# Optimization experiments

Measured on AMD Instinct MI355X. Metric: run time of the kernel, lower is better.

## Reference

```python
import jax, jax.numpy as jnp
import numpy as np

B, N, NC = 16, 25200, 80
CONF_THRES = 0.25
IOU_THRES = 0.45
MAX_DET = 300
MAX_WH = 7680.0   # yolov5 per-class box offset for class-aware NMS
TOPK = 1024       # pre-NMS candidate cap (fixed-shape stand-in for yolov5 max_nms)


def setup_inputs():
    key = jax.random.key(0)
    k1, k2 = jax.random.split(key)
    # xywh in pixel units (640x640 image, boxes up to ~120 px); obj/cls confidences in [0,1]
    xywh = jax.random.uniform(k1, (B, N, 4), dtype=jnp.float32) * jnp.array([640.0, 640.0, 120.0, 120.0], jnp.float32)
    conf = jax.random.uniform(k2, (B, N, 1 + NC), dtype=jnp.float32)
    return {"YOLOoutput": jnp.concatenate([xywh, conf], axis=-1)}


def _xywh2xyxy(x):
    cx, cy, w, h = x[..., 0], x[..., 1], x[..., 2], x[..., 3]
    return jnp.stack([cx - w / 2, cy - h / 2, cx + w / 2, cy + h / 2], axis=-1)


def _pairwise_iou(a, b):
    # a, b: [K,4] xyxy -> [K,K]
    lt = jnp.maximum(a[:, None, :2], b[None, :, :2])
    rb = jnp.minimum(a[:, None, 2:], b[None, :, 2:])
    wh = jnp.maximum(rb - lt, 0.0)
    inter = wh[..., 0] * wh[..., 1]
    area_a = (a[:, 2] - a[:, 0]) * (a[:, 3] - a[:, 1])
    area_b = (b[:, 2] - b[:, 0]) * (b[:, 3] - b[:, 1])
    return inter / (area_a[:, None] + area_b[None, :] - inter + 1e-7)


def _nms_single(pred):
    # pred: [N, 5+NC]
    obj = pred[:, 4]
    cls_conf = pred[:, 5:] * obj[:, None]      # conf = obj_conf * cls_conf (yolov5)
    conf = jnp.max(cls_conf, axis=-1)
    j = jnp.argmax(cls_conf, axis=-1)
    valid = (obj > CONF_THRES) & (conf > CONF_THRES)
    box = _xywh2xyxy(pred[:, :4])
    scores = jnp.where(valid, conf, -1.0)      # invalid candidates sink to bottom
    top_scores, idx = jax.lax.top_k(scores, TOPK)
    b = box[idx]                               # [TOPK,4]
    c = j[idx].astype(box.dtype)
    boxes_off = b + (c * MAX_WH)[:, None]      # class-aware NMS via per-class offset
    valid_k = top_scores > 0.0
    iou = _pairwise_iou(boxes_off, boxes_off)
    ar = jnp.arange(TOPK)

    def body(i, supp):
        active = jnp.logical_not(supp[i])
        return supp | (active & (iou[i] > IOU_THRES) & (ar > i))

    supp = jax.lax.fori_loop(0, TOPK, body, jnp.logical_not(valid_k))
    keep = valid_k & jnp.logical_not(supp)
    fs, fi = jax.lax.top_k(jnp.where(keep, top_scores, -1.0), MAX_DET)
    dv = fs > 0.0
    det_box = b[fi] * dv[:, None]              # zero out padded rows
    det = jnp.concatenate(
        [det_box, jnp.where(dv, fs, 0.0)[:, None], (c[fi] * dv)[:, None]], axis=-1
    )                                          # [MAX_DET, 6] = x1,y1,x2,y2,conf,cls
    return det, dv


def reference(YOLOoutput):
    det, dvalid = jax.vmap(_nms_single)(YOLOoutput)   # [B,MAX_DET,6], [B,MAX_DET]
    scores = det[..., 4]
    mean_conf = jnp.max(scores, axis=1)               # = 0 when image has no detections
    n = dvalid.sum(axis=1)
    terms = jnp.abs(det[..., 0:2] - det[..., 2:4]) * scores[..., None]  # padded rows are 0
    s = terms.sum(axis=(1, 2))
    wh = jnp.where(n > 0, s / (2.0 * jnp.maximum(n, 1)), 0.0)  # mean over n*2 elements
    conf_addition = mean_conf.sum() / B
    w_and_h = wh.sum() / B
    return conf_addition, w_and_h, det[2]
```

## Files before the change

### kernel.cpp

```cpp
#include <hip/hip_runtime.h>
#include <hip/hip_bf16.h>

typedef unsigned long long u64;
typedef unsigned int u32;

#define BATCH 16
#define NANCH 25200
#define NCLS 80
#define NFEAT 85
#define TOPK 1024
#define MAXDET 300
#define CONF_T 0.25f
#define IOU_T 0.45f
#define MAX_WH 7680.0f

#define GRP 16
#define GRPB (GRP * NFEAT * 4)
#define NGRP (NANCH / GRP)

__device__ __forceinline__ void gload_lds16(const void* g, void* l) {
    __builtin_amdgcn_global_load_lds(
        (const __attribute__((address_space(1))) unsigned int*)g,
        (__attribute__((address_space(3))) unsigned int*)l, 16, 0, 0);
}

__global__ __launch_bounds__(256) void score_kernel(const float* __restrict__ in,
                                                    u64* __restrict__ keys,
                                                    float* __restrict__ out) {
    __shared__ char lds[4 * GRPB];
    const int tid = threadIdx.x, wv = tid >> 6, lane = tid & 63;
    if (blockIdx.x == 0 && tid == 0) { out[0] = 0.0f; out[1] = 0.0f; }
    char* myl = lds + wv * GRPB;
    const float* myp = (const float*)myl + (lane >> 2) * NFEAT;
    const int a = lane >> 2, q = lane & 3;
    const int wave_id = (blockIdx.x << 2) | wv;
    const int nwaves = gridDim.x << 2;
    for (int g = wave_id; g < BATCH * NGRP; g += nwaves) {
        const int b = g / NGRP;
        const int a0 = (g - b * NGRP) * GRP;
        const char* gbase = (const char*)(in + ((size_t)b * NANCH + a0) * NFEAT);
#pragma unroll
        for (int r = 0; r < 6; ++r) {
            const int myb = (r << 10) + lane * 16;
            if (myb < GRPB) gload_lds16(gbase + myb, myl + (r << 10));
        }
        asm volatile("s_waitcnt vmcnt(0)" ::: "memory");
        __builtin_amdgcn_sched_barrier(0);
        float obj = myp[4];
        float best = -1e30f;
        int bj = 0;
#pragma unroll
        for (int k = 0; k < 20; ++k) {
            float v = myp[5 + q * 20 + k] * obj;
            if (v > best) { best = v; bj = q * 20 + k; }
        }
#pragma unroll
        for (int d = 1; d < 4; d <<= 1) {
            float ob = __shfl_xor(best, d, 64);
            int oj = __shfl_xor(bj, d, 64);
            if (ob > best || (ob == best && oj < bj)) { best = ob; bj = oj; }
        }
        if (q == 0) {
            bool valid = (obj > CONF_T) && (best > CONF_T);
            float sc = valid ? best : -1.0f;
            u32 sb = __float_as_uint(sc);
            u32 ord = sb ^ ((sb & 0x80000000u) ? 0xFFFFFFFFu : 0x80000000u);
            int idx = a0 + a;
            keys[(size_t)b * NANCH + idx] =
                ((u64)ord << 32) | ((u64)((u32)(idx ^ 0xFFFF) & 0xFFFFu) << 8) | (u64)bj;
        }
    }
}

__global__ __launch_bounds__(1024) void select_topk(const u64* __restrict__ keys,
                                                    const float* __restrict__ in,
                                                    float4* __restrict__ box4,
                                                    float4* __restrict__ boxoff4,
                                                    float* __restrict__ score,
                                                    float* __restrict__ cls,
                                                    u64* __restrict__ vmask) {
    const int b = blockIdx.x, tid = threadIdx.x;
    const int lane = tid & 63, wv = tid >> 6;
    const u64* kb = keys + (size_t)b * NANCH;
    const ulonglong2* kb2 = (const ulonglong2*)kb;
    __shared__ u32 wcnt[16][17];
    __shared__ u32 tot[17];
    __shared__ u32 s_prefix12, s_cnt;
    __shared__ u64 buf[2048];

    u32 myc = 0;
    for (int n = tid; n < 12600; n += 1024) {
        ulonglong2 kk = kb2[n];
        u32 b0 = (u32)(kk.x >> 52);
        u32 b1 = (u32)(kk.y >> 52);
        u32 c0 = (b0 == 0x407u) ? 16u : (b0 - 0xBE8u);
        u32 c1 = (b1 == 0x407u) ? 16u : (b1 - 0xBE8u);
#pragma unroll
        for (u32 k = 0; k < 17; ++k) {
            u64 m0 = __ballot(c0 == k);
            u64 m1 = __ballot(c1 == k);
            if (lane == (int)k) myc += (u32)__popcll(m0) + (u32)__popcll(m1);
        }
    }
    if (lane < 17) wcnt[wv][lane] = myc;
    if (tid == 0) s_cnt = 0u;
    __syncthreads();
    if (tid < 17) {
        u32 t = 0;
#pragma unroll
        for (int w = 0; w < 16; ++w) t += wcnt[w][tid];
        tot[tid] = t;
    }
    __syncthreads();
    if (tid == 0) {
        u32 acc = 0; u32 p = 0x407u;
        for (int k = 15; k >= 0; --k) {
            if (acc < (u32)TOPK && acc + tot[k] >= (u32)TOPK) p = 0xBE8u + (u32)k;
            acc += tot[k];
        }
        if (acc < (u32)TOPK) p = 0x407u;
        s_prefix12 = p;
    }
    __syncthreads();
    const u32 p12 = s_prefix12;
    for (int n = tid; n < 12600; n += 1024) {
        ulonglong2 kk = kb2[n];
        if ((u32)(kk.x >> 52) > p12) {
            u32 pos = atomicAdd(&s_cnt, 1u);
            if (pos < 2048u) buf[pos] = kk.x;
        }
        if ((u32)(kk.y >> 52) > p12) {
            u32 pos = atomicAdd(&s_cnt, 1u);
            if (pos < 2048u) buf[pos] = kk.y;
        }
    }
    __syncthreads();
    for (int n = tid; n < 12600; n += 1024) {
        ulonglong2 kk = kb2[n];
        if ((u32)(kk.x >> 52) == p12) {
            u32 pos = atomicAdd(&s_cnt, 1u);
            if (pos < 2048u) buf[pos] = kk.x;
        }
        if ((u32)(kk.y >> 52) == p12) {
            u32 pos = atomicAdd(&s_cnt, 1u);
            if (pos < 2048u) buf[pos] = kk.y;
        }
    }
    __syncthreads();
    u32 cnt = s_cnt; if (cnt > 2048u) cnt = 2048u;
    for (int n = (int)cnt + tid; n < 2048; n += 1024) buf[n] = 0ull;
    __syncthreads();

    const int base = wv * 128;
    u64 r0 = buf[base + lane], r1 = buf[base + 64 + lane];
    for (int k2 = 2; k2 <= 128; k2 <<= 1) {
        const bool d0 = (((base + lane) & k2) == 0);
        const bool d1 = (((base + 64 + lane) & k2) == 0);
        for (int jj = (k2 >> 1); jj >= 1; jj >>= 1) {
            if (jj == 64) {
                u64 mx = r0 > r1 ? r0 : r1, mn = r0 > r1 ? r1 : r0;
                r0 = d0 ? mx : mn; r1 = d0 ? mn : mx;
            } else {
                const bool up = (lane & jj) != 0;
                u64 v0 = __shfl_xor(r0, jj, 64);
                u64 v1 = __shfl_xor(r1, jj, 64);
                const bool km0 = (d0 != up), km1 = (d1 != up);
                r0 = km0 ? (r0 > v0 ? r0 : v0) : (r0 < v0 ? r0 : v0);
                r1 = km1 ? (r1 > v1 ? r1 : v1) : (r1 < v1 ? r1 : v1);
            }
        }
    }
    for (int k2 = 256; k2 <= 2048; k2 <<= 1) {
        buf[base + lane] = r0; buf[base + 64 + lane] = r1;
        __syncthreads();
        for (int jj = (k2 >> 1); jj >= 128; jj >>= 1) {
            int i = ((tid & ~(jj - 1)) << 1) | (tid & (jj - 1));
            int part = i | jj;
            u64 a = buf[i], c = buf[part];
            bool sw = ((i & k2) == 0) ? (a < c) : (a > c);
            if (sw) { buf[i] = c; buf[part] = a; }
            __syncthreads();
        }
        r0 = buf[base + lane]; r1 = buf[base + 64 + lane];
        const bool d0 = (((base + lane) & k2) == 0);
        for (int jj = 64; jj >= 1; jj >>= 1) {
            if (jj == 64) {
                u64 mx = r0 > r1 ? r0 : r1, mn = r0 > r1 ? r1 : r0;
                r0 = d0 ? mx : mn; r1 = d0 ? mn : mx;
            } else {
                const bool up = (lane & jj) != 0;
                u64 v0 = __shfl_xor(r0, jj, 64);
                u64 v1 = __shfl_xor(r1, jj, 64);
                const bool km = (d0 != up);
                r0 = km ? (r0 > v0 ? r0 : v0) : (r0 < v0 ? r0 : v0);
                r1 = km ? (r1 > v1 ? r1 : v1) : (r1 < v1 ? r1 : v1);
            }
        }
    }
    buf[base + lane] = r0; buf[base + 64 + lane] = r1;
    __syncthreads();

    u64 k = buf[tid];
    u32 ord = (u32)(k >> 32);
    u32 sb = (ord & 0x80000000u) ? (ord ^ 0x80000000u) : ~ord;
    float sc = __uint_as_float(sb);
    int idx = (int)((((u32)(k >> 8)) & 0xFFFFu) ^ 0xFFFFu);
    int j = (int)(k & 0xFFu);
    const float* pr = in + ((size_t)b * NANCH + idx) * NFEAT;
    float cx = pr[0], cy = pr[1], ww = pr[2], hh = pr[3];
    float x1 = cx - ww / 2.0f, y1 = cy - hh / 2.0f;
    float x2 = cx + ww / 2.0f, y2 = cy + hh / 2.0f;
    float c = (float)j;
    float cm = c * MAX_WH;
    box4[b * TOPK + tid]    = make_float4(x1, y1, x2, y2);
    boxoff4[b * TOPK + tid] = make_float4(x1 + cm, y1 + cm, x2 + cm, y2 + cm);
    score[b * TOPK + tid] = sc;
    cls[b * TOPK + tid] = c;
    u64 bal = __ballot(sc > 0.0f);
    if ((tid & 63) == 0) vmask[b * 16 + (tid >> 6)] = bal;
}

__global__ __launch_bounds__(256) void iou_mask(const float4* __restrict__ boxoff4,
                                                u64* __restrict__ M) {
    __shared__ float4 sbx[TOPK];
    const int b = blockIdx.x >> 8;
    const int rb = blockIdx.x & 255;
    const int i = (rb << 2) | (threadIdx.x >> 6);
    const int lane = threadIdx.x & 63;
    const int tw = rb >> 4;
    const int jmin = tw << 6;
    for (int t = jmin + threadIdx.x; t < TOPK; t += 256) sbx[t] = boxoff4[b * TOPK + t];
    __syncthreads();
    const float4 A = sbx[i];
    const float areaA = (A.z - A.x) * (A.w - A.y);
    u64 myword = 0ull;
#pragma unroll 4
    for (int t = tw; t < 16; ++t) {
        int j = (t << 6) | lane;
        float4 Bx = sbx[j];
        float lx = fmaxf(A.x, Bx.x), ly = fmaxf(A.y, Bx.y);
        float rx = fminf(A.z, Bx.z), ry = fminf(A.w, Bx.w);
        float iw = fmaxf(rx - lx, 0.0f), ih = fmaxf(ry - ly, 0.0f);
        float inter = iw * ih;
        float areaB = (Bx.z - Bx.x) * (Bx.w - Bx.y);
        float iou = inter / (areaA + areaB - inter + 1e-7f);
        bool pred = (iou > IOU_T) && (j > i);
        u64 bal = __ballot(pred);
        if (lane == t) myword = bal;
    }
    if (lane < 16) M[((size_t)b * TOPK + i) * 16 + lane] = myword;
}

__global__ __launch_bounds__(512) void nms_finalize(const u64* __restrict__ M,
                                                    const u64* __restrict__ vmask,
                                                    const float4* __restrict__ box4,
                                                    const float* __restrict__ score,
                                                    const float* __restrict__ cls,
                                                    float* __restrict__ out) {
    __shared__ u64 sM[TOPK * 16];
    __shared__ u64 kw[16];
    __shared__ int wpfx[17];
    __shared__ float sdet[MAXDET * 6];
    __shared__ float s_sum, s_max;
    const int b = blockIdx.x, tid = threadIdx.x;
    {
        const ulonglong2* Ms = (const ulonglong2*)(M + (size_t)b * TOPK * 16);
        ulonglong2* Ldst = (ulonglong2*)sM;
#pragma unroll 4
        for (int t = tid; t < TOPK * 8; t += 512) Ldst[t] = Ms[t];
    }
    for (int t = tid; t < MAXDET * 6; t += 512) sdet[t] = 0.0f;
    if (tid == 0) { s_sum = 0.0f; s_max = 0.0f; }
    __syncthreads();
    if (tid < 16) {
        const int w = tid;
        const u64 vm = vmask[b * 16 + w];
        u64 supp = ~vm;
        u64 rwA[16], rwB[16];
#pragma unroll
        for (int q = 0; q < 16; ++q) rwA[q] = sM[q * 16 + w];
        for (int wb = 0; wb < 16; ++wb) {
            u64 cur = __shfl(supp, wb, 64);
#pragma unroll
            for (int c4 = 0; c4 < 4; ++c4) {
                const int rn = wb * 64 + (c4 + 1) * 16;
                if (rn < 1024) {
#pragma unroll
                    for (int q = 0; q < 16; ++q) rwB[q] = sM[(rn + q) * 16 + w];
                }
                u64 rc[16];
#pragma unroll
                for (int q = 0; q < 16; ++q) rc[q] = __shfl(rwA[q], wb, 64);
                u64 ar0 = rc[0] | rc[4] | rc[8]  | rc[12];
                u64 ar1 = rc[1] | rc[5] | rc[9]  | rc[13];
                u64 ar2 = rc[2] | rc[6] | rc[10] | rc[14];
                u64 ar3 = rc[3] | rc[7] | rc[11] | rc[15];
                const u32 intra = (u32)(((ar0 | ar1) | (ar2 | ar3)) >> (c4 * 16)) & 0xFFFFu;
                const u32 actm  = (~(u32)(cur >> (c4 * 16))) & 0xFFFFu;
                if (intra == 0u || actm == 0u) {
                    u64 s0 = 0, s1 = 0, s2 = 0, s3 = 0;
                    u64 c0 = 0, c1 = 0, c2 = 0, c3 = 0;
#pragma unroll
                    for (int q = 0; q < 16; q += 4) {
                        const u64 m0 = ((actm >> (q + 0)) & 1u) ? ~0ull : 0ull;
                        const u64 m1 = ((actm >> (q + 1)) & 1u) ? ~0ull : 0ull;
                        const u64 m2 = ((actm >> (q + 2)) & 1u) ? ~0ull : 0ull;
                        const u64 m3 = ((actm >> (q + 3)) & 1u) ? ~0ull : 0ull;
                        s0 |= rwA[q + 0] & m0;  c0 |= rc[q + 0] & m0;
                        s1 |= rwA[q + 1] & m1;  c1 |= rc[q + 1] & m1;
                        s2 |= rwA[q + 2] & m2;  c2 |= rc[q + 2] & m2;
                        s3 |= rwA[q + 3] & m3;  c3 |= rc[q + 3] & m3;
                    }
                    supp |= (s0 | s1) | (s2 | s3);
                    cur  |= (c0 | c1) | (c2 | c3);
                } else {
#pragma unroll
                    for (int q = 0; q < 16; ++q) {
                        const int ii = c4 * 16 + q;
                        const bool act = ((cur >> ii) & 1ull) == 0ull;
                        supp = act ? (supp | rwA[q]) : supp;
                        cur  = act ? (cur  | rc[q])  : cur;
                    }
                }
#pragma unroll
                for (int q = 0; q < 16; ++q) rwA[q] = rwB[q];
            }
        }
        kw[w] = vm & ~supp;
    }
    __syncthreads();
    if (tid == 0) {
        int acc = 0;
        for (int w = 0; w < 16; ++w) { wpfx[w] = acc; acc += __popcll(kw[w]); }
        wpfx[16] = acc;
    }
    __syncthreads();
    for (int r = tid; r < TOPK; r += 512) {
        int w = r >> 6, bp = r & 63;
        if ((kw[w] >> bp) & 1ull) {
            int pos = wpfx[w] + __popcll(kw[w] & ((1ull << bp) - 1ull));
            if (pos < MAXDET) {
                float4 bx = box4[b * TOPK + r];
                float s = score[b * TOPK + r];
                float c = cls[b * TOPK + r];
                sdet[pos * 6 + 0] = bx.x;
                sdet[pos * 6 + 1] = bx.y;
                sdet[pos * 6 + 2] = bx.z;
                sdet[pos * 6 + 3] = bx.w;
                sdet[pos * 6 + 4] = s;
                sdet[pos * 6 + 5] = c;
                float term = (fabsf(bx.x - bx.z) + fabsf(bx.y - bx.w)) * s;
                atomicAdd(&s_sum, term);
                if (pos == 0) s_max = s;
            }
        }
    }
    __syncthreads();
    if (tid == 0) {
        int n = wpfx[16]; if (n > MAXDET) n = MAXDET;
        float wh = (n > 0) ? (s_sum / (2.0f * (float)n)) : 0.0f;
        atomicAdd(&out[0], s_max / (float)BATCH);
        atomicAdd(&out[1], wh / (float)BATCH);
    }
    if (b == 2) {
        for (int t = tid; t < MAXDET * 6; t += 512) out[2 + t] = sdet[t];
    }
}

extern "C" void kernel_launch(void* const* d_in, const int* in_sizes, int n_in,
                              void* d_out, int out_size, void* d_ws, size_t ws_size,
                              hipStream_t stream) {
    const float* in = (const float*)d_in[0];
    float* out = (float*)d_out;
    char* ws = (char*)d_ws;

    u64*    keys     = (u64*)   (ws + 0);
    float4* boxoff4  = (float4*)(ws + 3225600);
    float4* box4     = (float4*)(ws + 3487744);
    float*  score    = (float*) (ws + 3749888);
    float*  cls      = (float*) (ws + 3815424);
    u64*    vmask    = (u64*)   (ws + 3880960);
    u64*    M        = (u64*)   (ws + 3883008);

    score_kernel<<<2048, 256, 0, stream>>>(in, keys, out);
    select_topk<<<BATCH, 1024, 0, stream>>>(keys, in, box4, boxoff4, score, cls, vmask);
    iou_mask<<<BATCH * 256, 256, 0, stream>>>(boxoff4, M);
    nms_finalize<<<BATCH, 512, 0, stream>>>(M, vmask, box4, score, cls, out);
}
```

Baseline: 279.0 us.

## Fuse select, IoU mask and NMS stages into one cooperative kernel

Replaces the three launches after scoring (top-k select, IoU mask, NMS finalize) with a single cooperative kernel of 256 blocks of 1024 threads that separates the stages with grid-wide syncs. Shared memory is overlaid through a union of the per-stage layouts. The aim is to remove kernel launch gaps and inter-kernel drain between stages. In exchange, the IoU stage runs on fewer, larger blocks, and the grid syncs plus a 1024-thread NMS block add overhead. The score kernel grid is also changed from 2048 to 2100 blocks.

Result: slower. 484.3 us (+73.6%).

```diff
diff --git a/kernel.cpp b/kernel.cpp
--- a/kernel.cpp
+++ b/kernel.cpp
@@ -1,5 +1,5 @@
 #include <hip/hip_runtime.h>
-#include <hip/hip_bf16.h>
+#include <hip/hip_cooperative_groups.h>
 
 typedef unsigned long long u64;
 typedef unsigned int u32;
@@ -72,21 +72,34 @@
     }
 }
 
-__global__ __launch_bounds__(1024) void select_topk(const u64* __restrict__ keys,
-                                                    const float* __restrict__ in,
-                                                    float4* __restrict__ box4,
-                                                    float4* __restrict__ boxoff4,
-                                                    float* __restrict__ score,
-                                                    float* __restrict__ cls,
-                                                    u64* __restrict__ vmask) {
-    const int b = blockIdx.x, tid = threadIdx.x;
+struct SmemS {
+    u32 wcnt[16][17];
+    u32 tot[17];
+    u32 s_prefix12, s_cnt;
+    u64 buf[2048];
+};
+struct SmemI { float4 sbx[TOPK]; };
+struct SmemN {
+    u64 sM[TOPK * 16];
+    u64 kw[16];
+    int wpfx[17];
+    float sdet[MAXDET * 6];
+    float s_sum, s_max;
+};
+union SmemU { SmemS s; SmemI i; SmemN n; };
+
+__device__ __forceinline__ void dev_select(int b, int tid, SmemS& sm,
+                                           const u64* __restrict__ keys,
+                                           const float* __restrict__ in,
+                                           float4* __restrict__ box4,
+                                           float4* __restrict__ boxoff4,
+                                           float* __restrict__ score,
+                                           float* __restrict__ cls,
+                                           u64* __restrict__ vmask) {
     const int lane = tid & 63, wv = tid >> 6;
     const u64* kb = keys + (size_t)b * NANCH;
     const ulonglong2* kb2 = (const ulonglong2*)kb;
-    __shared__ u32 wcnt[16][17];
-    __shared__ u32 tot[17];
-    __shared__ u32 s_prefix12, s_cnt;
-    __shared__ u64 buf[2048];
+    u64* buf = sm.buf;
 
     u32 myc = 0;
     for (int n = tid; n < 12600; n += 1024) {
@@ -102,35 +115,35 @@
             if (lane == (int)k) myc += (u32)__popcll(m0) + (u32)__popcll(m1);
         }
     }
-    if (lane < 17) wcnt[wv][lane] = myc;
-    if (tid == 0) s_cnt = 0u;
+    if (lane < 17) sm.wcnt[wv][lane] = myc;
+    if (tid == 0) sm.s_cnt = 0u;
     __syncthreads();
     if (tid < 17) {
         u32 t = 0;
 #pragma unroll
-        for (int w = 0; w < 16; ++w) t += wcnt[w][tid];
-        tot[tid] = t;
+        for (int w = 0; w < 16; ++w) t += sm.wcnt[w][tid];
+        sm.tot[tid] = t;
     }
     __syncthreads();
     if (tid == 0) {
         u32 acc = 0; u32 p = 0x407u;
         for (int k = 15; k >= 0; --k) {
-            if (acc < (u32)TOPK && acc + tot[k] >= (u32)TOPK) p = 0xBE8u + (u32)k;
-            acc += tot[k];
+            if (acc < (u32)TOPK && acc + sm.tot[k] >= (u32)TOPK) p = 0xBE8u + (u32)k;
+            acc += sm.tot[k];
         }
         if (acc < (u32)TOPK) p = 0x407u;
-        s_prefix12 = p;
-    }
-    __syncthreads();
-    const u32 p12 = s_prefix12;
+        sm.s_prefix12 = p;
+    }
+    __syncthreads();
+    const u32 p12 = sm.s_prefix12;
     for (int n = tid; n < 12600; n += 1024) {
         ulonglong2 kk = kb2[n];
         if ((u32)(kk.x >> 52) > p12) {
-            u32 pos = atomicAdd(&s_cnt, 1u);
+            u32 pos = atomicAdd(&sm.s_cnt, 1u);
             if (pos < 2048u) buf[pos] = kk.x;
         }
         if ((u32)(kk.y >> 52) > p12) {
-            u32 pos = atomicAdd(&s_cnt, 1u);
+            u32 pos = atomicAdd(&sm.s_cnt, 1u);
             if (pos < 2048u) buf[pos] = kk.y;
         }
     }
@@ -138,16 +151,16 @@
     for (int n = tid; n < 12600; n += 1024) {
         ulonglong2 kk = kb2[n];
         if ((u32)(kk.x >> 52) == p12) {
-            u32 pos = atomicAdd(&s_cnt, 1u);
+            u32 pos = atomicAdd(&sm.s_cnt, 1u);
             if (pos < 2048u) buf[pos] = kk.x;
         }
         if ((u32)(kk.y >> 52) == p12) {
-            u32 pos = atomicAdd(&s_cnt, 1u);
+            u32 pos = atomicAdd(&sm.s_cnt, 1u);
             if (pos < 2048u) buf[pos] = kk.y;
         }
     }
     __syncthreads();
-    u32 cnt = s_cnt; if (cnt > 2048u) cnt = 2048u;
+    u32 cnt = sm.s_cnt; if (cnt > 2048u) cnt = 2048u;
     for (int n = (int)cnt + tid; n < 2048; n += 1024) buf[n] = 0ull;
     __syncthreads();
 
@@ -220,6 +233,182 @@
     if ((tid & 63) == 0) vmask[b * 16 + (tid >> 6)] = bal;
 }
 
+__device__ __forceinline__ void dev_nms(int b, int tid, int stride, SmemN& sm,
+                                        const u64* __restrict__ M,
+                                        const u64* __restrict__ vmask,
+                                        const float4* __restrict__ box4,
+                                        const float* __restrict__ score,
+                                        const float* __restrict__ cls,
+                                        float* __restrict__ out) {
+    {
+        const ulonglong2* Ms = (const ulonglong2*)(M + (size_t)b * TOPK * 16);
+        ulonglong2* Ldst = (ulonglong2*)sm.sM;
+#pragma unroll 4
+        for (int t = tid; t < TOPK * 8; t += stride) Ldst[t] = Ms[t];
+    }
+    for (int t = tid; t < MAXDET * 6; t += stride) sm.sdet[t] = 0.0f;
+    if (tid == 0) { sm.s_sum = 0.0f; sm.s_max = 0.0f; }
+    __syncthreads();
+    if (tid < 16) {
+        const int w = tid;
+        const u64 vm = vmask[b * 16 + w];
+        u64 supp = ~vm;
+        u64 rwA[16], rwB[16];
+#pragma unroll
+        for (int q = 0; q < 16; ++q) rwA[q] = sm.sM[q * 16 + w];
+        for (int wb = 0; wb < 16; ++wb) {
+            u64 cur = __shfl(supp, wb, 64);
+#pragma unroll
+            for (int c4 = 0; c4 < 4; ++c4) {
+                const int rn = wb * 64 + (c4 + 1) * 16;
+                if (rn < 1024) {
+#pragma unroll
+                    for (int q = 0; q < 16; ++q) rwB[q] = sm.sM[(rn + q) * 16 + w];
+                }
+                u64 rc[16];
+#pragma unroll
+                for (int q = 0; q < 16; ++q) rc[q] = __shfl(rwA[q], wb, 64);
+                u64 ar0 = rc[0] | rc[4] | rc[8]  | rc[12];
+                u64 ar1 = rc[1] | rc[5] | rc[9]  | rc[13];
+                u64 ar2 = rc[2] | rc[6] | rc[10] | rc[14];
+                u64 ar3 = rc[3] | rc[7] | rc[11] | rc[15];
+                const u32 intra = (u32)(((ar0 | ar1) | (ar2 | ar3)) >> (c4 * 16)) & 0xFFFFu;
+                const u32 actm  = (~(u32)(cur >> (c4 * 16))) & 0xFFFFu;
+                if (intra == 0u || actm == 0u) {
+                    u64 s0 = 0, s1 = 0, s2 = 0, s3 = 0;
+                    u64 c0 = 0, c1 = 0, c2 = 0, c3 = 0;
+#pragma unroll
+                    for (int q = 0; q < 16; q += 4) {
+                        const u64 m0 = ((actm >> (q + 0)) & 1u) ? ~0ull : 0ull;
+                        const u64 m1 = ((actm >> (q + 1)) & 1u) ? ~0ull : 0ull;
+                        const u64 m2 = ((actm >> (q + 2)) & 1u) ? ~0ull : 0ull;
+                        const u64 m3 = ((actm >> (q + 3)) & 1u) ? ~0ull : 0ull;
+                        s0 |= rwA[q + 0] & m0;  c0 |= rc[q + 0] & m0;
+                        s1 |= rwA[q + 1] & m1;  c1 |= rc[q + 1] & m1;
+                        s2 |= rwA[q + 2] & m2;  c2 |= rc[q + 2] & m2;
+                        s3 |= rwA[q + 3] & m3;  c3 |= rc[q + 3] & m3;
+                    }
+                    supp |= (s0 | s1) | (s2 | s3);
+                    cur  |= (c0 | c1) | (c2 | c3);
+                } else {
+#pragma unroll
+                    for (int q = 0; q < 16; ++q) {
+                        const int ii = c4 * 16 + q;
+                        const bool act = ((cur >> ii) & 1ull) == 0ull;
+                        supp = act ? (supp | rwA[q]) : supp;
+                        cur  = act ? (cur  | rc[q])  : cur;
+                    }
+                }
+#pragma unroll
+                for (int q = 0; q < 16; ++q) rwA[q] = rwB[q];
+            }
+        }
+        sm.kw[w] = vm & ~supp;
+    }
+    __syncthreads();
+    if (tid == 0) {
+        int acc = 0;
+        for (int w = 0; w < 16; ++w) { sm.wpfx[w] = acc; acc += __popcll(sm.kw[w]); }
+        sm.wpfx[16] = acc;
+    }
+    __syncthreads();
+    for (int r = tid; r < TOPK; r += stride) {
+        int w = r >> 6, bp = r & 63;
+        if ((sm.kw[w] >> bp) & 1ull) {
+            int pos = sm.wpfx[w] + __popcll(sm.kw[w] & ((1ull << bp) - 1ull));
+            if (pos < MAXDET) {
+                float4 bx = box4[b * TOPK + r];
+                float s = score[b * TOPK + r];
+                float c = cls[b * TOPK + r];
+                sm.sdet[pos * 6 + 0] = bx.x;
+                sm.sdet[pos * 6 + 1] = bx.y;
+                sm.sdet[pos * 6 + 2] = bx.z;
+                sm.sdet[pos * 6 + 3] = bx.w;
+                sm.sdet[pos * 6 + 4] = s;
+                sm.sdet[pos * 6 + 5] = c;
+                float term = (fabsf(bx.x - bx.z) + fabsf(bx.y - bx.w)) * s;
+                atomicAdd(&sm.s_sum, term);
+                if (pos == 0) sm.s_max = s;
+            }
+        }
+    }
+    __syncthreads();
+    if (tid == 0) {
+        int n = sm.wpfx[16]; if (n > MAXDET) n = MAXDET;
+        float wh = (n > 0) ? (sm.s_sum / (2.0f * (float)n)) : 0.0f;
+        atomicAdd(&out[0], sm.s_max / (float)BATCH);
+        atomicAdd(&out[1], wh / (float)BATCH);
+    }
+    if (b == 2) {
+        for (int t = tid; t < MAXDET * 6; t += stride) out[2 + t] = sm.sdet[t];
+    }
+}
+
+__global__ __launch_bounds__(1024) void coop_pipeline(const u64* __restrict__ keys,
+                                                      const float* __restrict__ in,
+                                                      float4* __restrict__ box4,
+                                                      float4* __restrict__ boxoff4,
+                                                      float* __restrict__ score,
+                                                      float* __restrict__ cls,
+                                                      u64* __restrict__ vmask,
+                                                      u64* __restrict__ M,
+                                                      float* __restrict__ out) {
+    __shared__ SmemU u;
+    cooperative_groups::grid_group grid = cooperative_groups::this_grid();
+    const int tid = threadIdx.x;
+
+    if (blockIdx.x < BATCH)
+        dev_select(blockIdx.x, tid, u.s, keys, in, box4, boxoff4, score, cls, vmask);
+    __threadfence();
+    grid.sync();
+
+    {
+        const int bb = blockIdx.x >> 4;
+        const int rquad = blockIdx.x & 15;
+        const int jmin = rquad << 6;
+        for (int t = jmin + tid; t < TOPK; t += 1024) u.i.sbx[t] = boxoff4[bb * TOPK + t];
+        __syncthreads();
+        const int wv = tid >> 6, lane = tid & 63;
+#pragma unroll
+        for (int s = 0; s < 4; ++s) {
+            const int i = (rquad << 6) + (s << 4) + wv;
+            const float4 A = u.i.sbx[i];
+            const float areaA = (A.z - A.x) * (A.w - A.y);
+            u64 myword = 0ull;
+            for (int t = rquad; t < 16; ++t) {
+                int j = (t << 6) | lane;
+                float4 Bx = u.i.sbx[j];
+                float lx = fmaxf(A.x, Bx.x), ly = fmaxf(A.y, Bx.y);
+                float rx = fminf(A.z, Bx.z), ry = fminf(A.w, Bx.w);
+                float iw = fmaxf(rx - lx, 0.0f), ih = fmaxf(ry - ly, 0.0f);
+                float inter = iw * ih;
+                float areaB = (Bx.z - Bx.x) * (Bx.w - Bx.y);
+                float iou = inter / (areaA + areaB - inter + 1e-7f);
+                bool pred = (iou > IOU_T) && (j > i);
+                u64 bal = __ballot(pred);
+                if (lane == t) myword = bal;
+            }
+            if (lane < 16) M[((size_t)bb * TOPK + i) * 16 + lane] = myword;
+        }
+    }
+    __threadfence();
+    grid.sync();
+
+    if (blockIdx.x < BATCH)
+        dev_nms(blockIdx.x, tid, 1024, u.n, M, vmask, box4, score, cls, out);
+}
+
+__global__ __launch_bounds__(1024) void select_topk_k(const u64* __restrict__ keys,
+                                                      const float* __restrict__ in,
+                                                      float4* __restrict__ box4,
+                                                      float4* __restrict__ boxoff4,
+                                                      float* __restrict__ score,
+                                                      float* __restrict__ cls,
+                                                      u64* __restrict__ vmask) {
+    __shared__ SmemS sm;
+    dev_select(blockIdx.x, threadIdx.x, sm, keys, in, box4, boxoff4, score, cls, vmask);
+}
+
 __global__ __launch_bounds__(256) void iou_mask(const float4* __restrict__ boxoff4,
                                                 u64* __restrict__ M) {
     __shared__ float4 sbx[TOPK];
@@ -251,120 +440,14 @@
     if (lane < 16) M[((size_t)b * TOPK + i) * 16 + lane] = myword;
 }
 
-__global__ __launch_bounds__(512) void nms_finalize(const u64* __restrict__ M,
-                                                    const u64* __restrict__ vmask,
-                                                    const float4* __restrict__ box4,
-                                                    const float* __restrict__ score,
-                                                    const float* __restrict__ cls,
-                                                    float* __restrict__ out) {
-    __shared__ u64 sM[TOPK * 16];
-    __shared__ u64 kw[16];
-    __shared__ int wpfx[17];
-    __shared__ float sdet[MAXDET * 6];
-    __shared__ float s_sum, s_max;
-    const int b = blockIdx.x, tid = threadIdx.x;
-    {
-        const ulonglong2* Ms = (const ulonglong2*)(M + (size_t)b * TOPK * 16);
-        ulonglong2* Ldst = (ulonglong2*)sM;
-#pragma unroll 4
-        for (int t = tid; t < TOPK * 8; t += 512) Ldst[t] = Ms[t];
-    }
-    for (int t = tid; t < MAXDET * 6; t += 512) sdet[t] = 0.0f;
-    if (tid == 0) { s_sum = 0.0f; s_max = 0.0f; }
-    __syncthreads();
-    if (tid < 16) {
-        const int w = tid;
-        const u64 vm = vmask[b * 16 + w];
-        u64 supp = ~vm;
-        u64 rwA[16], rwB[16];
-#pragma unroll
-        for (int q = 0; q < 16; ++q) rwA[q] = sM[q * 16 + w];
-        for (int wb = 0; wb < 16; ++wb) {
-            u64 cur = __shfl(supp, wb, 64);
-#pragma unroll
-            for (int c4 = 0; c4 < 4; ++c4) {
-                const int rn = wb * 64 + (c4 + 1) * 16;
-                if (rn < 1024) {
-#pragma unroll
-                    for (int q = 0; q < 16; ++q) rwB[q] = sM[(rn + q) * 16 + w];
-                }
-                u64 rc[16];
-#pragma unroll
-                for (int q = 0; q < 16; ++q) rc[q] = __shfl(rwA[q], wb, 64);
-                u64 ar0 = rc[0] | rc[4] | rc[8]  | rc[12];
-                u64 ar1 = rc[1] | rc[5] | rc[9]  | rc[13];
-                u64 ar2 = rc[2] | rc[6] | rc[10] | rc[14];
-                u64 ar3 = rc[3] | rc[7] | rc[11] | rc[15];
-                const u32 intra = (u32)(((ar0 | ar1) | (ar2 | ar3)) >> (c4 * 16)) & 0xFFFFu;
-                const u32 actm  = (~(u32)(cur >> (c4 * 16))) & 0xFFFFu;
-                if (intra == 0u || actm == 0u) {
-                    u64 s0 = 0, s1 = 0, s2 = 0, s3 = 0;
-                    u64 c0 = 0, c1 = 0, c2 = 0, c3 = 0;
-#pragma unroll
-                    for (int q = 0; q < 16; q += 4) {
-                        const u64 m0 = ((actm >> (q + 0)) & 1u) ? ~0ull : 0ull;
-                        const u64 m1 = ((actm >> (q + 1)) & 1u) ? ~0ull : 0ull;
-                        const u64 m2 = ((actm >> (q + 2)) & 1u) ? ~0ull : 0ull;
-                        const u64 m3 = ((actm >> (q + 3)) & 1u) ? ~0ull : 0ull;
-                        s0 |= rwA[q + 0] & m0;  c0 |= rc[q + 0] & m0;
-                        s1 |= rwA[q + 1] & m1;  c1 |= rc[q + 1] & m1;
-                        s2 |= rwA[q + 2] & m2;  c2 |= rc[q + 2] & m2;
-                        s3 |= rwA[q + 3] & m3;  c3 |= rc[q + 3] & m3;
-                    }
-                    supp |= (s0 | s1) | (s2 | s3);
-                    cur  |= (c0 | c1) | (c2 | c3);
-                } else {
-#pragma unroll
-                    for (int q = 0; q < 16; ++q) {
-                        const int ii = c4 * 16 + q;
-                        const bool act = ((cur >> ii) & 1ull) == 0ull;
-                        supp = act ? (supp | rwA[q]) : supp;
-                        cur  = act ? (cur  | rc[q])  : cur;
-                    }
-                }
-#pragma unroll
-                for (int q = 0; q < 16; ++q) rwA[q] = rwB[q];
-            }
-        }
-        kw[w] = vm & ~supp;
-    }
-    __syncthreads();
-    if (tid == 0) {
-        int acc = 0;
-        for (int w = 0; w < 16; ++w) { wpfx[w] = acc; acc += __popcll(kw[w]); }
-        wpfx[16] = acc;
-    }
-    __syncthreads();
-    for (int r = tid; r < TOPK; r += 512) {
-        int w = r >> 6, bp = r & 63;
-        if ((kw[w] >> bp) & 1ull) {
-            int pos = wpfx[w] + __popcll(kw[w] & ((1ull << bp) - 1ull));
-            if (pos < MAXDET) {
-                float4 bx = box4[b * TOPK + r];
-                float s = score[b * TOPK + r];
-                float c = cls[b * TOPK + r];
-                sdet[pos * 6 + 0] = bx.x;
-                sdet[pos * 6 + 1] = bx.y;
-                sdet[pos * 6 + 2] = bx.z;
-                sdet[pos * 6 + 3] = bx.w;
-                sdet[pos * 6 + 4] = s;
-                sdet[pos * 6 + 5] = c;
-                float term = (fabsf(bx.x - bx.z) + fabsf(bx.y - bx.w)) * s;
-                atomicAdd(&s_sum, term);
-                if (pos == 0) s_max = s;
-            }
-        }
-    }
-    __syncthreads();
-    if (tid == 0) {
-        int n = wpfx[16]; if (n > MAXDET) n = MAXDET;
-        float wh = (n > 0) ? (s_sum / (2.0f * (float)n)) : 0.0f;
-        atomicAdd(&out[0], s_max / (float)BATCH);
-        atomicAdd(&out[1], wh / (float)BATCH);
-    }
-    if (b == 2) {
-        for (int t = tid; t < MAXDET * 6; t += 512) out[2 + t] = sdet[t];
-    }
+__global__ __launch_bounds__(512) void nms_finalize_k(const u64* __restrict__ M,
+                                                      const u64* __restrict__ vmask,
+                                                      const float4* __restrict__ box4,
+                                                      const float* __restrict__ score,
+                                                      const float* __restrict__ cls,
+                                                      float* __restrict__ out) {
+    __shared__ SmemN sm;
+    dev_nms(blockIdx.x, threadIdx.x, 512, sm, M, vmask, box4, score, cls, out);
 }
 
 extern "C" void kernel_launch(void* const* d_in, const int* in_sizes, int n_in,
@@ -382,8 +465,25 @@
     u64*    vmask    = (u64*)   (ws + 3880960);
     u64*    M        = (u64*)   (ws + 3883008);
 
-    score_kernel<<<2048, 256, 0, stream>>>(in, keys, out);
-    select_topk<<<BATCH, 1024, 0, stream>>>(keys, in, box4, boxoff4, score, cls, vmask);
-    iou_mask<<<BATCH * 256, 256, 0, stream>>>(boxoff4, M);
-    nms_finalize<<<BATCH, 512, 0, stream>>>(M, vmask, box4, score, cls, out);
-}
+    static int s_coop = -1;
+    if (s_coop < 0) {
+        int dev = 0; hipGetDevice(&dev);
+        int v = 0;
+        hipDeviceGetAttribute(&v, hipDeviceAttributeCooperativeLaunch, dev);
+        s_coop = v;
+    }
+
+    score_kernel<<<2100, 256, 0, stream>>>(in, keys, out);
+
+    if (s_coop) {
+        void* args[] = { (void*)&keys, (void*)&in, (void*)&box4, (void*)&boxoff4,
+                         (void*)&score, (void*)&cls, (void*)&vmask, (void*)&M,
+                         (void*)&out };
+        hipLaunchCooperativeKernel((const void*)coop_pipeline, dim3(256), dim3(1024),
+                                   args, 0, stream);
+    } else {
+        select_topk_k<<<BATCH, 1024, 0, stream>>>(keys, in, box4, boxoff4, score, cls, vmask);
+        iou_mask<<<BATCH * 256, 256, 0, stream>>>(boxoff4, M);
+        nms_finalize_k<<<BATCH, 512, 0, stream>>>(M, vmask, box4, score, cls, out);
+    }
+}
```

## Double-buffer score kernel global-to-LDS loads and shrink its grid

Applied to the files above, without the earlier changes.

The score kernel now keeps two LDS slots per wave. It issues the direct global-to-LDS loads for the next anchor group before computing the current one, so memory latency overlaps with the class max and argmax work. The grid drops from 2048 to 768 blocks so each wave loops over more groups and the prefetch has something to overlap. The cost is double the LDS per block and fewer resident blocks, which could reduce latency hiding from occupancy. It also relies on hand-written vmcnt and lgkmcnt waits, which must match the number of issued loads.

Result: no change. 277.3 us (-0.6%).

```diff
diff --git a/kernel.cpp b/kernel.cpp
--- a/kernel.cpp
+++ b/kernel.cpp
@@ -27,25 +27,49 @@
 __global__ __launch_bounds__(256) void score_kernel(const float* __restrict__ in,
                                                     u64* __restrict__ keys,
                                                     float* __restrict__ out) {
-    __shared__ char lds[4 * GRPB];
+    __shared__ char lds[8 * GRPB];
     const int tid = threadIdx.x, wv = tid >> 6, lane = tid & 63;
     if (blockIdx.x == 0 && tid == 0) { out[0] = 0.0f; out[1] = 0.0f; }
-    char* myl = lds + wv * GRPB;
-    const float* myp = (const float*)myl + (lane >> 2) * NFEAT;
+    char* sl0 = lds + wv * (2 * GRPB);
+    char* sl1 = sl0 + GRPB;
     const int a = lane >> 2, q = lane & 3;
     const int wave_id = (blockIdx.x << 2) | wv;
     const int nwaves = gridDim.x << 2;
-    for (int g = wave_id; g < BATCH * NGRP; g += nwaves) {
+    const int total = BATCH * NGRP;
+
+    char* cur = sl0;
+    char* nxt = sl1;
+    {
+        const int g = wave_id;
         const int b = g / NGRP;
         const int a0 = (g - b * NGRP) * GRP;
         const char* gbase = (const char*)(in + ((size_t)b * NANCH + a0) * NFEAT);
 #pragma unroll
         for (int r = 0; r < 6; ++r) {
             const int myb = (r << 10) + lane * 16;
-            if (myb < GRPB) gload_lds16(gbase + myb, myl + (r << 10));
-        }
-        asm volatile("s_waitcnt vmcnt(0)" ::: "memory");
+            if (myb < GRPB) gload_lds16(gbase + myb, cur + (r << 10));
+        }
+    }
+    for (int g = wave_id; g < total; g += nwaves) {
+        const int gn = g + nwaves;
+        if (gn < total) {
+            const int bn = gn / NGRP;
+            const int an0 = (gn - bn * NGRP) * GRP;
+            const char* gb = (const char*)(in + ((size_t)bn * NANCH + an0) * NFEAT);
+            asm volatile("s_waitcnt lgkmcnt(0)" ::: "memory");
+#pragma unroll
+            for (int r = 0; r < 6; ++r) {
+                const int myb = (r << 10) + lane * 16;
+                if (myb < GRPB) gload_lds16(gb + myb, nxt + (r << 10));
+            }
+            asm volatile("s_waitcnt vmcnt(6)" ::: "memory");
+        } else {
+            asm volatile("s_waitcnt vmcnt(0)" ::: "memory");
+        }
         __builtin_amdgcn_sched_barrier(0);
+        const int b = g / NGRP;
+        const int a0 = (g - b * NGRP) * GRP;
+        const float* myp = (const float*)cur + a * NFEAT;
         float obj = myp[4];
         float best = -1e30f;
         int bj = 0;
@@ -69,6 +93,7 @@
             keys[(size_t)b * NANCH + idx] =
                 ((u64)ord << 32) | ((u64)((u32)(idx ^ 0xFFFF) & 0xFFFFu) << 8) | (u64)bj;
         }
+        char* t = cur; cur = nxt; nxt = t;
     }
 }
 
@@ -382,7 +407,7 @@
     u64*    vmask    = (u64*)   (ws + 3880960);
     u64*    M        = (u64*)   (ws + 3883008);
 
-    score_kernel<<<2048, 256, 0, stream>>>(in, keys, out);
+    score_kernel<<<768, 256, 0, stream>>>(in, keys, out);
     select_topk<<<BATCH, 1024, 0, stream>>>(keys, in, box4, boxoff4, score, cls, vmask);
     iou_mask<<<BATCH * 256, 256, 0, stream>>>(boxoff4, M);
     nms_finalize<<<BATCH, 512, 0, stream>>>(M, vmask, box4, score, cls, out);
```
